# Performance work log

Measured on AMD Instinct MI355X. Metric: run time of the kernel, lower is better.

Reference implementation:

```python
import jax, jax.numpy as jnp
import numpy as np

NUM_HEADS = 4
HEAD_DIM = 64  # out_dim // num_heads = 256 // 4
NEG_SLOPE = 0.2


def setup_inputs() -> dict:
    key = jax.random.key(0)
    k1, k2 = jax.random.split(key)
    h = jax.random.normal(k1, (8, 2048, 256), dtype=jnp.float32)
    # Linear(in_dim, head_dim*num_heads, bias=False): store as [in_dim, out_dim]
    W = jax.random.normal(k2, (256, 256), dtype=jnp.float32) * (1.0 / np.sqrt(256.0))
    return {"h": h, "W": W}


def reference(h, W):
    B, T, _ = h.shape
    # Wh: (B, H, T, D)
    Wh = (h @ W).reshape(B, T, NUM_HEADS, HEAD_DIM).transpose(0, 2, 1, 3)
    scale = 1.0 / (HEAD_DIM ** 0.5)
    # full T x T scores per head, LeakyReLU then softmax over keys
    scores = jnp.einsum('bhtd,bhsd->bhts', Wh, Wh) * scale
    attention = jax.nn.softmax(jax.nn.leaky_relu(scores, negative_slope=NEG_SLOPE), axis=-1)
    h_prime = jnp.einsum('bhts,bhsd->bhtd', attention, Wh)
    # concat=True: (B, T, H*D)
    return h_prime.transpose(0, 2, 1, 3).reshape(B, T, NUM_HEADS * HEAD_DIM)
```

## Files before the change

### kernel.cpp

```cpp
#include <hip/hip_runtime.h>

#define T_SEQ 2048
#define NH 4
#define DH 64

typedef __bf16 bf16x8 __attribute__((ext_vector_type(8)));
typedef float f32x4 __attribute__((ext_vector_type(4)));
typedef unsigned short u16x8 __attribute__((ext_vector_type(8)));

__device__ __forceinline__ unsigned short f2bf_rne(float x) {
  unsigned int u = __builtin_bit_cast(unsigned int, x);
  u += 0x7fffu + ((u >> 16) & 1u);
  return (unsigned short)(u >> 16);
}

__device__ __forceinline__ void async_cp16(const unsigned short* g, unsigned short* l) {
  __builtin_amdgcn_global_load_lds(
      (const __attribute__((address_space(1))) unsigned int*)g,
      (__attribute__((address_space(3))) unsigned int*)l, 16, 0, 0);
}

__global__ __launch_bounds__(256) void wprep(const float* __restrict__ W,
                                             unsigned short* __restrict__ Wt) {
  int tid = blockIdx.x * 256 + threadIdx.x;
  int k = tid >> 8, n = tid & 255;
  float w = W[tid];
  unsigned int u = __builtin_bit_cast(unsigned int, w);
  Wt[n * 256 + k] = (unsigned short)(u >> 16);
  float lo = w - __builtin_bit_cast(float, u & 0xffff0000u);
  Wt[65536 + n * 256 + k] =
      (unsigned short)(__builtin_bit_cast(unsigned int, lo) >> 16);
}

__global__ __launch_bounds__(256, 2) void wh_gemm(
    const float* __restrict__ h, const unsigned short* __restrict__ Wt,
    unsigned short* __restrict__ Kb, unsigned short* __restrict__ Vt) {
  __shared__ __align__(16) unsigned short Ahi[32 * 256];
  __shared__ __align__(16) unsigned short Alo[32 * 256];
  const int tid = threadIdx.x;
  const int wave = tid >> 6;
  const int lane = tid & 63;
  const int l15 = lane & 15;
  const int quad = lane >> 4;
  const int mbase = blockIdx.x * 32;
  const int col0 = wave * 64;

  {
    const int r = tid >> 3;
    const int cbase = (tid & 7) * 4;
    const float4* hp = (const float4*)(h + ((size_t)(mbase + r) << 8) + cbase * 8);
#pragma unroll
    for (int j = 0; j < 4; j++) {
      float4 f0 = hp[2 * j];
      float4 f1 = hp[2 * j + 1];
      u16x8 hi, lo;
#define SPLIT1(v, idx)                                                    \
  {                                                                       \
    unsigned int u_ = __builtin_bit_cast(unsigned int, (v));              \
    hi[idx] = (unsigned short)(u_ >> 16);                                 \
    float r_ = (v) - __builtin_bit_cast(float, u_ & 0xffff0000u);         \
    lo[idx] = (unsigned short)(__builtin_bit_cast(unsigned int, r_) >> 16); \
  }
      SPLIT1(f0.x, 0) SPLIT1(f0.y, 1) SPLIT1(f0.z, 2) SPLIT1(f0.w, 3)
      SPLIT1(f1.x, 4) SPLIT1(f1.y, 5) SPLIT1(f1.z, 6) SPLIT1(f1.w, 7)
#undef SPLIT1
      const int chunk = (cbase + j) ^ (r & 7);
      *(u16x8*)&Ahi[r * 256 + chunk * 8] = hi;
      *(u16x8*)&Alo[r * 256 + chunk * 8] = lo;
    }
  }
  __syncthreads();

  f32x4 acc[2][4];
#pragma unroll
  for (int mt = 0; mt < 2; mt++)
#pragma unroll
    for (int nt = 0; nt < 4; nt++) acc[mt][nt] = (f32x4){0.f, 0.f, 0.f, 0.f};

#pragma unroll 2
  for (int ks = 0; ks < 8; ks++) {
    const int k0 = ks * 32 + quad * 8;
    bf16x8 ahi[2], alo[2];
#pragma unroll
    for (int mt = 0; mt < 2; mt++) {
      const int row = mt * 16 + l15;
      const int ch = (ks * 4 + quad) ^ (row & 7);
      ahi[mt] = *(const bf16x8*)&Ahi[row * 256 + ch * 8];
      alo[mt] = *(const bf16x8*)&Alo[row * 256 + ch * 8];
    }
#pragma unroll
    for (int nt = 0; nt < 4; nt++) {
      const unsigned short* wp = Wt + ((size_t)(col0 + nt * 16 + l15) << 8) + k0;
      bf16x8 bhi = *(const bf16x8*)wp;
      bf16x8 blo = *(const bf16x8*)(wp + 65536);
#pragma unroll
      for (int mt = 0; mt < 2; mt++) {
        acc[mt][nt] = __builtin_amdgcn_mfma_f32_16x16x32_bf16(ahi[mt], bhi, acc[mt][nt], 0, 0, 0);
        acc[mt][nt] = __builtin_amdgcn_mfma_f32_16x16x32_bf16(alo[mt], bhi, acc[mt][nt], 0, 0, 0);
        acc[mt][nt] = __builtin_amdgcn_mfma_f32_16x16x32_bf16(ahi[mt], blo, acc[mt][nt], 0, 0, 0);
      }
    }
  }

  const float s1 = 0.424664717f;
#pragma unroll
  for (int mt = 0; mt < 2; mt++) {
    int row = mbase + mt * 16 + quad * 4;
    int b = row >> 11;
    int tb = row & 2047;
    size_t bh = (size_t)(b * NH + wave);
#pragma unroll
    for (int nt = 0; nt < 4; nt++) {
      int d = nt * 16 + l15;
      Kb[(bh * T_SEQ + tb + 0) * DH + d] = f2bf_rne(acc[mt][nt][0] * s1);
      Kb[(bh * T_SEQ + tb + 1) * DH + d] = f2bf_rne(acc[mt][nt][1] * s1);
      Kb[(bh * T_SEQ + tb + 2) * DH + d] = f2bf_rne(acc[mt][nt][2] * s1);
      Kb[(bh * T_SEQ + tb + 3) * DH + d] = f2bf_rne(acc[mt][nt][3] * s1);
      ushort4 vp;
      vp.x = f2bf_rne(acc[mt][nt][0]);
      vp.y = f2bf_rne(acc[mt][nt][1]);
      vp.z = f2bf_rne(acc[mt][nt][2]);
      vp.w = f2bf_rne(acc[mt][nt][3]);
      *(ushort4*)&Vt[(bh * DH + d) * T_SEQ + tb] = vp;
    }
  }
}

__global__ __launch_bounds__(256, 3) void attn(
    const unsigned short* __restrict__ Kb, const unsigned short* __restrict__ Vt,
    float* __restrict__ out) {
  __shared__ __align__(16) unsigned short ldsK[2][64 * 64];
  __shared__ __align__(16) unsigned short ldsV[2][64 * 64];
  __shared__ __align__(16) unsigned short ldsP[4][32 * 64];
  const int tid = threadIdx.x;
  const int wave = tid >> 6;
  const int lane = tid & 63;
  const int l15 = lane & 15;
  const int quad = lane >> 4;
  const int lbid = (blockIdx.x & 7) * 64 + (blockIdx.x >> 3);
  const int bh = lbid >> 4;
  const int qtile = lbid & 15;
  const unsigned short* Kbh = Kb + (size_t)bh * T_SEQ * DH;
  const unsigned short* Vbh = Vt + (size_t)bh * DH * T_SEQ;

  const int qbase = qtile * 128 + wave * 32;
  bf16x8 aq[2][2];
#pragma unroll
  for (int mt = 0; mt < 2; mt++) {
    const unsigned short* qp = &Kbh[(qbase + mt * 16 + l15) * DH + quad * 8];
    aq[mt][0] = *(const bf16x8*)qp;
    aq[mt][1] = *(const bf16x8*)(qp + 32);
  }

  f32x4 o[2][4];
  float lsum[2][4];
#pragma unroll
  for (int mt = 0; mt < 2; mt++)
#pragma unroll
    for (int i = 0; i < 4; i++) {
      o[mt][i] = (f32x4){0.f, 0.f, 0.f, 0.f};
      lsum[mt][i] = 0.f;
    }
  unsigned short* Pw = ldsP[wave];

  auto stage = [&](int t, int buf) {
#pragma unroll
    for (int i = 0; i < 2; i++) {
      int slot = i * 256 + tid;
      int r = slot >> 3;
      int c = (slot & 7) ^ (r & 7);
      async_cp16(&Kbh[(t * 64 + r) * DH + c * 8],
                 &ldsK[buf][(i * 256 + wave * 64) * 8]);
      async_cp16(&Vbh[(size_t)r * T_SEQ + t * 64 + c * 8],
                 &ldsV[buf][(i * 256 + wave * 64) * 8]);
    }
  };

  stage(0, 0);

  for (int kt = 0; kt < 32; kt++) {
    const int cur = kt & 1;
    if (kt < 31) {
      stage(kt + 1, cur ^ 1);
      asm volatile("s_waitcnt vmcnt(4)" ::: "memory");
    } else {
      asm volatile("s_waitcnt vmcnt(0)" ::: "memory");
    }
    __builtin_amdgcn_s_barrier();
    __builtin_amdgcn_sched_barrier(0);

    const unsigned short* Kl = ldsK[cur];
    const unsigned short* Vl = ldsV[cur];

    f32x4 sfr[2][4];
    __builtin_amdgcn_s_setprio(1);
#pragma unroll
    for (int nt = 0; nt < 4; nt++) {
      int key = nt * 16 + l15;
      bf16x8 kf0 = *(const bf16x8*)&Kl[key * 64 + ((quad ^ (key & 7)) << 3)];
      bf16x8 kf1 = *(const bf16x8*)&Kl[key * 64 + (((4 + quad) ^ (key & 7)) << 3)];
#pragma unroll
      for (int mt = 0; mt < 2; mt++) {
        f32x4 s = {0.f, 0.f, 0.f, 0.f};
        s = __builtin_amdgcn_mfma_f32_16x16x32_bf16(aq[mt][0], kf0, s, 0, 0, 0);
        s = __builtin_amdgcn_mfma_f32_16x16x32_bf16(aq[mt][1], kf1, s, 0, 0, 0);
        sfr[mt][nt] = s;
      }
    }
    __builtin_amdgcn_s_setprio(0);

#pragma unroll
    for (int mt = 0; mt < 2; mt++)
#pragma unroll
      for (int nt = 0; nt < 4; nt++) {
        int col = nt * 16 + l15;
#pragma unroll
        for (int reg = 0; reg < 4; reg++) {
          float v = sfr[mt][nt][reg];
          float e = __builtin_amdgcn_exp2f(fmaxf(v, 0.2f * v));
          lsum[mt][reg] += e;
          int row = mt * 16 + quad * 4 + reg;
          Pw[(row << 6) + (((((col >> 3) ^ (row & 7))) << 3) | (col & 7))] =
              (unsigned short)(__builtin_bit_cast(unsigned int, e) >> 16);
        }
      }
    __builtin_amdgcn_s_waitcnt(0xC07F);

    __builtin_amdgcn_s_setprio(1);
#pragma unroll
    for (int kc = 0; kc < 2; kc++) {
      const int pch = (((kc << 2) + quad) ^ (l15 & 7)) << 3;
      bf16x8 ap0 = *(const bf16x8*)&Pw[(l15 << 6) + pch];
      bf16x8 ap1 = *(const bf16x8*)&Pw[((16 + l15) << 6) + pch];
#pragma unroll
      for (int nt = 0; nt < 4; nt++) {
        int d = nt * 16 + l15;
        bf16x8 vf = *(const bf16x8*)&Vl[(d << 6) + ((((kc << 2) + quad) ^ (d & 7)) << 3)];
        o[0][nt] = __builtin_amdgcn_mfma_f32_16x16x32_bf16(ap0, vf, o[0][nt], 0, 0, 0);
        o[1][nt] = __builtin_amdgcn_mfma_f32_16x16x32_bf16(ap1, vf, o[1][nt], 0, 0, 0);
      }
    }
    __builtin_amdgcn_s_setprio(0);
    __builtin_amdgcn_sched_barrier(0);
    __builtin_amdgcn_s_barrier();
  }

  const int b = bh >> 2, head = bh & 3;
#pragma unroll
  for (int mt = 0; mt < 2; mt++) {
    float inv[4];
#pragma unroll
    for (int reg = 0; reg < 4; reg++) {
      float l = lsum[mt][reg];
      l += __shfl_xor(l, 1, 64);
      l += __shfl_xor(l, 2, 64);
      l += __shfl_xor(l, 4, 64);
      l += __shfl_xor(l, 8, 64);
      inv[reg] = 1.0f / l;
    }
#pragma unroll
    for (int nt = 0; nt < 4; nt++) {
      int d = nt * 16 + l15;
#pragma unroll
      for (int reg = 0; reg < 4; reg++) {
        int trow = qbase + mt * 16 + quad * 4 + reg;
        out[((size_t)b * T_SEQ + trow) * 256 + head * 64 + d] = o[mt][nt][reg] * inv[reg];
      }
    }
  }
}

extern "C" void kernel_launch(void* const* d_in, const int* in_sizes, int n_in,
                              void* d_out, int out_size, void* d_ws, size_t ws_size,
                              hipStream_t stream) {
  const float* h = (const float*)d_in[0];
  const float* W = (const float*)d_in[1];
  float* out = (float*)d_out;
  unsigned short* Kb = (unsigned short*)d_ws;
  unsigned short* Vt = Kb + (size_t)32 * T_SEQ * DH;
  unsigned short* Wt = Vt + (size_t)32 * T_SEQ * DH;
  wprep<<<256, 256, 0, stream>>>(W, Wt);
  wh_gemm<<<512, 256, 0, stream>>>(h, Wt, Kb, Vt);
  attn<<<512, 256, 0, stream>>>(Kb, Vt, out);
}
```

Measured before the change: 149.3 us.

## Software-pipeline QK^T of next tile with softmax and PV of previous

Restructures the attention key loop so each step computes the QK^T scores for tile t while doing softmax and the PV MFMAs for tile t-1. Two score register sets alternate between steps, and V is now triple-buffered in LDS. The aim is to overlap exp/LDS-store softmax work with matrix-core work and hide the dependency stall between QK and PV. The extra live registers are paid for by lowering the launch-bounds occupancy hint from 3 to 2 blocks per CU. There is also a possible race: no barrier separates the prologue's qkt(0) from the first step's stage(2), which overwrites K buffer 0.

```diff
diff --git a/kernel.cpp b/kernel.cpp
--- a/kernel.cpp
+++ b/kernel.cpp
@@ -126,12 +126,12 @@
   }
 }
 
-__global__ __launch_bounds__(256, 3) void attn(
+__global__ __launch_bounds__(256, 2) void attn(
     const unsigned short* __restrict__ Kb, const unsigned short* __restrict__ Vt,
     float* __restrict__ out) {
-  __shared__ __align__(16) unsigned short ldsK[2][64 * 64];
-  __shared__ __align__(16) unsigned short ldsV[2][64 * 64];
-  __shared__ __align__(16) unsigned short ldsP[4][32 * 64];
+  __shared__ __align__(16) unsigned short ldsK[2 * 4096];
+  __shared__ __align__(16) unsigned short ldsV[3 * 4096];
+  __shared__ __align__(16) unsigned short ldsP[4][2048];
   const int tid = threadIdx.x;
   const int wave = tid >> 6;
   const int lane = tid & 63;
@@ -163,36 +163,21 @@
     }
   unsigned short* Pw = ldsP[wave];
 
-  auto stage = [&](int t, int buf) {
+  auto stage = [&](int t) {
+    unsigned short* kb = ldsK + (t & 1) * 4096;
+    unsigned short* vb = ldsV + (t % 3) * 4096;
 #pragma unroll
     for (int i = 0; i < 2; i++) {
       int slot = i * 256 + tid;
       int r = slot >> 3;
       int c = (slot & 7) ^ (r & 7);
-      async_cp16(&Kbh[(t * 64 + r) * DH + c * 8],
-                 &ldsK[buf][(i * 256 + wave * 64) * 8]);
-      async_cp16(&Vbh[(size_t)r * T_SEQ + t * 64 + c * 8],
-                 &ldsV[buf][(i * 256 + wave * 64) * 8]);
-    }
-  };
-
-  stage(0, 0);
-
-  for (int kt = 0; kt < 32; kt++) {
-    const int cur = kt & 1;
-    if (kt < 31) {
-      stage(kt + 1, cur ^ 1);
-      asm volatile("s_waitcnt vmcnt(4)" ::: "memory");
-    } else {
-      asm volatile("s_waitcnt vmcnt(0)" ::: "memory");
-    }
-    __builtin_amdgcn_s_barrier();
-    __builtin_amdgcn_sched_barrier(0);
-
-    const unsigned short* Kl = ldsK[cur];
-    const unsigned short* Vl = ldsV[cur];
-
-    f32x4 sfr[2][4];
+      async_cp16(&Kbh[(t * 64 + r) * DH + c * 8], kb + (i * 256 + wave * 64) * 8);
+      async_cp16(&Vbh[(size_t)r * T_SEQ + t * 64 + c * 8], vb + (i * 256 + wave * 64) * 8);
+    }
+  };
+
+  auto qkt = [&](int t, f32x4 (&sfr)[2][4]) {
+    const unsigned short* Kl = ldsK + (t & 1) * 4096;
     __builtin_amdgcn_s_setprio(1);
 #pragma unroll
     for (int nt = 0; nt < 4; nt++) {
@@ -208,7 +193,9 @@
       }
     }
     __builtin_amdgcn_s_setprio(0);
-
+  };
+
+  auto softmax = [&](f32x4 (&sfr)[2][4]) {
 #pragma unroll
     for (int mt = 0; mt < 2; mt++)
 #pragma unroll
@@ -224,8 +211,10 @@
               (unsigned short)(__builtin_bit_cast(unsigned int, e) >> 16);
         }
       }
-    __builtin_amdgcn_s_waitcnt(0xC07F);
-
+  };
+
+  auto pv = [&](int t) {
+    const unsigned short* Vl = ldsV + (t % 3) * 4096;
     __builtin_amdgcn_s_setprio(1);
 #pragma unroll
     for (int kc = 0; kc < 2; kc++) {
@@ -241,9 +230,40 @@
       }
     }
     __builtin_amdgcn_s_setprio(0);
+  };
+
+  f32x4 sfrA[2][4], sfrB[2][4];
+
+  stage(0);
+  stage(1);
+  asm volatile("s_waitcnt vmcnt(4)" ::: "memory");
+  __builtin_amdgcn_s_barrier();
+  __builtin_amdgcn_sched_barrier(0);
+  qkt(0, sfrB);
+
+  auto step = [&](int t, f32x4 (&sn)[2][4], f32x4 (&so)[2][4], bool has_next) {
+    if (has_next) {
+      stage(t + 1);
+      asm volatile("s_waitcnt vmcnt(4)" ::: "memory");
+    } else {
+      asm volatile("s_waitcnt vmcnt(0)" ::: "memory");
+    }
+    __builtin_amdgcn_s_barrier();
+    __builtin_amdgcn_sched_barrier(0);
+    if (t <= 31) qkt(t, sn);
+    softmax(so);
+    __builtin_amdgcn_s_waitcnt(0xC07F);
+    pv(t - 1);
     __builtin_amdgcn_sched_barrier(0);
     __builtin_amdgcn_s_barrier();
-  }
+  };
+
+  for (int it = 1; it < 31; it += 2) {
+    step(it, sfrA, sfrB, true);
+    step(it + 1, sfrB, sfrA, true);
+  }
+  step(31, sfrA, sfrB, false);
+  step(32, sfrB, sfrA, false);
 
   const int b = bh >> 2, head = bh & 3;
 #pragma unroll
```

Measured after the change: 150.3 us. No clear change (+0.7%).
